# Optimization experiments

Measured on AMD Instinct MI355X. Metric: run time of the kernel, lower is better.

Reference implementation:

```python
import jax, jax.numpy as jnp
import numpy as np
from jax import lax

B, T, C, H, W = 8, 2048, 128, 256, 16
LN_EPS = 1e-5


def setup_inputs() -> dict:
    key = jax.random.key(0)
    ks = jax.random.split(key, 8)
    s_ih = 1.0 / np.sqrt(H)
    return {
        "x": jax.random.normal(ks[0], (B, T, C), jnp.float32),
        "w_ih": jax.random.uniform(ks[1], (3 * H, C), jnp.float32, -s_ih, s_ih),
        "w_hh": jax.random.uniform(ks[2], (3 * H, H), jnp.float32, -s_ih, s_ih),
        "b_ih": jax.random.uniform(ks[3], (3 * H,), jnp.float32, -s_ih, s_ih),
        "b_hh": jax.random.uniform(ks[4], (3 * H,), jnp.float32, -s_ih, s_ih),
        "w_proj": jax.random.normal(ks[5], (H, H), jnp.float32) * (1.0 / np.sqrt(H)),
        "b_proj": jnp.zeros((H,), jnp.float32),
        "ln_gamma": jnp.ones((H,), jnp.float32),
        "ln_beta": jnp.zeros((H,), jnp.float32),
    }


def _sliding_gru(x, w_ih, w_hh, b_ih, b_hh):
    # x: [B,T,C]. Equivalent to running a GRU over each length-W left-padded
    # window ending at t, for all t, returning the final hidden state [B,T,H].
    pad = W - 1
    x_pad = jnp.pad(x, ((0, 0), (pad, 0), (0, 0)))  # [B, T+W-1, C]
    # Precompute input projection once (avoids the [B,T,W,C] unfold buffer).
    xi = jnp.einsum("btc,gc->btg", x_pad, w_ih) + b_ih  # [B, T+W-1, 3H]

    def step(h, w):
        # window step w sees x_pad[:, w : w+T, :] -> precomputed gates slice
        gi = lax.dynamic_slice_in_dim(xi, w, T, axis=1)  # [B,T,3H]
        gh = jnp.einsum("bth,gh->btg", h, w_hh) + b_hh   # [B,T,3H]
        gi_r, gi_z, gi_n = jnp.split(gi, 3, axis=-1)
        gh_r, gh_z, gh_n = jnp.split(gh, 3, axis=-1)
        r = jax.nn.sigmoid(gi_r + gh_r)
        z = jax.nn.sigmoid(gi_z + gh_z)
        n = jnp.tanh(gi_n + r * gh_n)
        h_new = (1.0 - z) * n + z * h
        return h_new, None

    h0 = jnp.zeros((B, T, H), x.dtype)
    h_final, _ = lax.scan(step, h0, jnp.arange(W))
    return h_final  # [B,T,H]


def reference(x, w_ih, w_hh, b_ih, b_hh, w_proj, b_proj, ln_gamma, ln_beta):
    feats = _sliding_gru(x, w_ih, w_hh, b_ih, b_hh)  # [B,T,H]
    y = jnp.einsum("bth,oh->bto", feats, w_proj) + b_proj
    mu = jnp.mean(y, axis=-1, keepdims=True)
    var = jnp.mean(jnp.square(y - mu), axis=-1, keepdims=True)
    y = (y - mu) * lax.rsqrt(var + LN_EPS) * ln_gamma + ln_beta
    return jax.nn.gelu(y, approximate=False)  # dropout is identity in eval
```

## Files before the change

kernel.cpp:

```cpp
#include <hip/hip_runtime.h>
#include <math.h>

typedef unsigned short u16;
typedef unsigned int   u32;
typedef __attribute__((ext_vector_type(8)))  short short8;
typedef __attribute__((ext_vector_type(16))) float f32x16;

#define NT 2048
#define NC 128
#define NH 256
#define NW 16
#define TPAD 2063

#define WS_GI_OFF 720896
#define WS_NEEDED (WS_GI_OFF + (size_t)8 * TPAD * 256 * 8)

__device__ __forceinline__ u16 f2bf(float f) {
  u32 u = __builtin_bit_cast(u32, f);
  u = u + 0x7fffu + ((u >> 16) & 1u);
  return (u16)(u >> 16);
}
__device__ __forceinline__ float bf2f(u16 v) {
  return __builtin_bit_cast(float, (u32)v << 16);
}
__device__ __forceinline__ float bflo(u32 w) {
  return __builtin_bit_cast(float, w << 16);
}
__device__ __forceinline__ float bfhi(u32 w) {
  return __builtin_bit_cast(float, w & 0xffff0000u);
}
__device__ __forceinline__ float nclamp(float v) {
  return fminf(fmaxf(v, -30.0f), 30.0f);
}
__device__ __forceinline__ float fsig(float x) {
  return __builtin_amdgcn_rcpf(1.0f + __builtin_amdgcn_exp2f(-1.44269504f * x));
}
__device__ __forceinline__ float ftanhf(float x) {
  float e = __builtin_amdgcn_exp2f(2.88539008f * x);
  return 1.0f - 2.0f * __builtin_amdgcn_rcpf(e + 1.0f);
}
__device__ __forceinline__ float gelu(float v) {
  return 0.5f * v * (1.0f + erff(v * 0.70710678118654752f));
}

__global__ void pack_w(const float* __restrict__ whh, const float* __restrict__ wih,
                       const float* __restrict__ wpr,
                       u16* __restrict__ whh_p, u16* __restrict__ wih_p,
                       u16* __restrict__ wpr_p) {
  int t = blockIdx.x * 256 + threadIdx.x;
  u16 v[8];
  if (t < 24576) {
    int lane = t & 63, kit = (t >> 6) & 15, nt = t >> 10;
    int wv = nt / 3, g = nt - wv * 3;
    int grow = g * 256 + wv * 32 + (lane & 31);
    int kb = kit * 16 + (lane >> 5) * 8;
    #pragma unroll
    for (int e = 0; e < 8; ++e) v[e] = f2bf(whh[grow * 256 + kb + e]);
    u32* d = (u32*)(whh_p + (size_t)t * 8);
    #pragma unroll
    for (int e = 0; e < 4; ++e) d[e] = (u32)v[2*e] | ((u32)v[2*e+1] << 16);
  } else if (t < 36864) {
    int t2 = t - 24576;
    int lane = t2 & 63, kit = (t2 >> 6) & 7, nt = t2 >> 9;
    int wv = nt / 3, g = nt - wv * 3;
    int grow = g * 256 + wv * 32 + (lane & 31);
    int kb = kit * 16 + (lane >> 5) * 8;
    #pragma unroll
    for (int e = 0; e < 8; ++e) v[e] = f2bf(wih[grow * 128 + kb + e]);
    u32* d = (u32*)(wih_p + (size_t)t2 * 8);
    #pragma unroll
    for (int e = 0; e < 4; ++e) d[e] = (u32)v[2*e] | ((u32)v[2*e+1] << 16);
  } else if (t < 45056) {
    int t3 = t - 36864;
    int lane = t3 & 63, kit = (t3 >> 6) & 15, nt = t3 >> 10;
    int o = nt * 32 + (lane & 31);
    int kb = kit * 16 + (lane >> 5) * 8;
    #pragma unroll
    for (int e = 0; e < 8; ++e) v[e] = f2bf(wpr[o * 256 + kb + e]);
    u32* d = (u32*)(wpr_p + (size_t)t3 * 8);
    #pragma unroll
    for (int e = 0; e < 4; ++e) d[e] = (u32)v[2*e] | ((u32)v[2*e+1] << 16);
  }
}

__global__ __launch_bounds__(512, 2) void xi_kernel(
    const float* __restrict__ x, const float* __restrict__ b_ih,
    const u16* __restrict__ wih_p, uint2* __restrict__ gi) {
  __shared__ u16 xs[64 * 128];
  const int tid = threadIdx.x, wv = tid >> 6, lane = tid & 63;
  const int ml = lane & 31, lh = lane >> 5;
  const int b = blockIdx.x / 33, chunk = blockIdx.x % 33;
  const int tp0 = chunk * 64;
  const int j = wv * 32 + ml;

  {
    int r = tid >> 3, c0e = (tid & 7) * 16;
    int xr = tp0 + r - (NW - 1);
    float vv[16];
    if (xr >= 0 && xr < NT) {
      const float4* src = (const float4*)(x + ((long)b * NT + xr) * NC + c0e);
      #pragma unroll
      for (int q = 0; q < 4; ++q) {
        float4 f = src[q];
        vv[q*4+0] = f.x; vv[q*4+1] = f.y; vv[q*4+2] = f.z; vv[q*4+3] = f.w;
      }
    } else {
      #pragma unroll
      for (int q = 0; q < 16; ++q) vv[q] = 0.0f;
    }
    int byb = r * 256 + c0e * 2;
    int sw = (r & 15) << 4;
    #pragma unroll
    for (int ch = 0; ch < 2; ++ch) {
      u32 q0 = (u32)f2bf(vv[ch*8+0]) | ((u32)f2bf(vv[ch*8+1]) << 16);
      u32 q1 = (u32)f2bf(vv[ch*8+2]) | ((u32)f2bf(vv[ch*8+3]) << 16);
      u32 q2 = (u32)f2bf(vv[ch*8+4]) | ((u32)f2bf(vv[ch*8+5]) << 16);
      u32 q3 = (u32)f2bf(vv[ch*8+6]) | ((u32)f2bf(vv[ch*8+7]) << 16);
      *(uint4*)((char*)xs + ((byb + ch * 16) ^ sw)) = make_uint4(q0, q1, q2, q3);
    }
  }
  __syncthreads();

  const float bi0 = b_ih[j], bi1 = b_ih[NH + j], bi2 = b_ih[2 * NH + j];
  f32x16 acc[2][3];
  #pragma unroll
  for (int mt = 0; mt < 2; ++mt) {
    #pragma unroll
    for (int e = 0; e < 16; ++e) {
      acc[mt][0][e] = bi0; acc[mt][1][e] = bi1; acc[mt][2][e] = bi2;
    }
  }

  const int sw0 = (ml & 15) << 4;
  #pragma unroll 4
  for (int kit = 0; kit < 8; ++kit) {
    short8 a0 = *(const short8*)((const char*)xs +
                  ((ml * 256 + kit * 32 + lh * 16) ^ sw0));
    short8 a1 = *(const short8*)((const char*)xs +
                  (((ml + 32) * 256 + kit * 32 + lh * 16) ^ sw0));
    #pragma unroll
    for (int g = 0; g < 3; ++g) {
      short8 bfr = __builtin_bit_cast(short8,
                     ((const uint4*)wih_p)[((wv * 3 + g) * 8 + kit) * 64 + lane]);
      acc[0][g] = __builtin_amdgcn_mfma_f32_32x32x16_bf16(a0, bfr, acc[0][g], 0, 0, 0);
      acc[1][g] = __builtin_amdgcn_mfma_f32_32x32x16_bf16(a1, bfr, acc[1][g], 0, 0, 0);
    }
  }

  #pragma unroll
  for (int mt = 0; mt < 2; ++mt) {
    #pragma unroll
    for (int rg = 0; rg < 16; ++rg) {
      int m = mt * 32 + (rg & 3) + 8 * (rg >> 2) + 4 * lh;
      int tp = tp0 + m;
      if (tp < TPAD) {
        u32 rz = (u32)f2bf(acc[mt][0][rg]) | ((u32)f2bf(acc[mt][1][rg]) << 16);
        u32 nn = (u32)f2bf(acc[mt][2][rg]);
        gi[((long)b * TPAD + tp) * 256 + j] = make_uint2(rz, nn);
      }
    }
  }
}

__global__ __launch_bounds__(512, 2) void gru_main(
    const float* __restrict__ b_hh,
    const u16* __restrict__ whh_p, const u16* __restrict__ wpr_p,
    const uint2* __restrict__ gi,
    const float* __restrict__ c256_0, const float* __restrict__ c256_1,
    const float* __restrict__ c256_2, float* __restrict__ out) {
  __shared__ u32 rz_lds[79 * 256];
  __shared__ u16 n_lds[79 * 256];
  __shared__ u16 hbuf[64 * 256];
  const int tid = threadIdx.x, wv = tid >> 6, lane = tid & 63;
  const int ml = lane & 31, lh = lane >> 5;
  const int wg = (blockIdx.x & 7) * 32 + (blockIdx.x >> 3);
  const int bidx = wg >> 5, t0 = (wg & 31) * 64;
  const long R0 = (long)wg * 64;
  const int j = wv * 32 + ml;

  const float *gp, *bpp, *bep;
  {
    float v0 = c256_0[0], v1 = c256_1[0];
    if (fabsf(v0 - 1.0f) < 0.25f)      { gp = c256_0; bpp = c256_1; bep = c256_2; }
    else if (fabsf(v1 - 1.0f) < 0.25f) { gp = c256_1; bpp = c256_0; bep = c256_2; }
    else                               { gp = c256_2; bpp = c256_0; bep = c256_1; }
  }

  const float bhr = b_hh[j], bhz = b_hh[NH + j], bnh = b_hh[2 * NH + j];

  {
    const uint2* gwin = gi + ((long)bidx * TPAD + t0) * 256;
    for (int idx = tid; idx < 79 * 256; idx += 512) {
      uint2 v = gwin[idx];
      rz_lds[idx] = v.x;
      n_lds[idx] = (u16)v.y;
    }
  }
  __syncthreads();

  float hreg[2][16];
  #pragma unroll
  for (int mt = 0; mt < 2; ++mt)
    #pragma unroll
    for (int rg = 0; rg < 16; ++rg) hreg[mt][rg] = 0.0f;

  const int swh = (ml & 15) << 4;

  for (int s = 0; s < NW; ++s) {
    f32x16 acc[2][3];
    #pragma unroll
    for (int mt = 0; mt < 2; ++mt) {
      #pragma unroll
      for (int e = 0; e < 16; ++e) {
        acc[mt][0][e] = bhr; acc[mt][1][e] = bhz; acc[mt][2][e] = bnh;
      }
    }

    if (s > 0) {
      #pragma unroll 4
      for (int kit = 0; kit < 16; ++kit) {
        short8 a0 = *(const short8*)((const char*)hbuf +
                      ((ml * 512 + kit * 32 + lh * 16) ^ swh));
        short8 a1 = *(const short8*)((const char*)hbuf +
                      (((ml + 32) * 512 + kit * 32 + lh * 16) ^ swh));
        #pragma unroll
        for (int g = 0; g < 3; ++g) {
          short8 bfr = __builtin_bit_cast(short8,
                         ((const uint4*)whh_p)[(((wv * 3 + g) * 16) + kit) * 64 + lane]);
          acc[0][g] = __builtin_amdgcn_mfma_f32_32x32x16_bf16(a0, bfr, acc[0][g], 0, 0, 0);
          acc[1][g] = __builtin_amdgcn_mfma_f32_32x32x16_bf16(a1, bfr, acc[1][g], 0, 0, 0);
        }
      }
    }
    __syncthreads();

    #pragma unroll
    for (int mt = 0; mt < 2; ++mt) {
      #pragma unroll
      for (int rg = 0; rg < 16; ++rg) {
        int m = mt * 32 + (rg & 3) + 8 * (rg >> 2) + 4 * lh;
        int ro = (s + m) * 256 + j;
        u32 rzv = rz_lds[ro];
        float gnv = bf2f(n_lds[ro]);
        float r = fsig(nclamp(bflo(rzv) + acc[mt][0][rg]));
        float z = fsig(nclamp(bfhi(rzv) + acc[mt][1][rg]));
        float n = ftanhf(nclamp(gnv + r * acc[mt][2][rg]));
        float hv = n + z * (hreg[mt][rg] - n);
        hreg[mt][rg] = hv;
        *(u16*)((char*)hbuf + ((m * 512 + j * 2) ^ ((m & 15) << 4))) = f2bf(hv);
      }
    }
    __syncthreads();
  }

  f32x16 pc[2];
  #pragma unroll
  for (int mt = 0; mt < 2; ++mt)
    #pragma unroll
    for (int e = 0; e < 16; ++e) pc[mt][e] = 0.0f;
  #pragma unroll 4
  for (int kit = 0; kit < 16; ++kit) {
    short8 a0 = *(const short8*)((const char*)hbuf +
                  ((ml * 512 + kit * 32 + lh * 16) ^ swh));
    short8 a1 = *(const short8*)((const char*)hbuf +
                  (((ml + 32) * 512 + kit * 32 + lh * 16) ^ swh));
    short8 bfr = __builtin_bit_cast(short8,
                   ((const uint4*)wpr_p)[(wv * 16 + kit) * 64 + lane]);
    pc[0] = __builtin_amdgcn_mfma_f32_32x32x16_bf16(a0, bfr, pc[0], 0, 0, 0);
    pc[1] = __builtin_amdgcn_mfma_f32_32x32x16_bf16(a1, bfr, pc[1], 0, 0, 0);
  }
  const float bp = bpp[j];
  __syncthreads();
  #pragma unroll
  for (int mt = 0; mt < 2; ++mt) {
    #pragma unroll
    for (int rg = 0; rg < 16; ++rg) {
      int m = mt * 32 + (rg & 3) + 8 * (rg >> 2) + 4 * lh;
      *(u16*)((char*)hbuf + ((m * 512 + j * 2) ^ ((m & 15) << 4))) = f2bf(pc[mt][rg] + bp);
    }
  }
  __syncthreads();

  {
    int m = tid >> 3, cg = (tid & 7) * 32;
    int sw = (m & 15) << 4;
    float v[32];
    #pragma unroll
    for (int q = 0; q < 4; ++q) {
      uint4 raw = *(const uint4*)((char*)hbuf + ((m * 512 + cg * 2 + q * 16) ^ sw));
      u32 w4[4] = {raw.x, raw.y, raw.z, raw.w};
      #pragma unroll
      for (int e = 0; e < 4; ++e) {
        v[q * 8 + e * 2]     = bflo(w4[e]);
        v[q * 8 + e * 2 + 1] = bfhi(w4[e]);
      }
    }
    float s1 = 0.0f, s2 = 0.0f;
    #pragma unroll
    for (int i = 0; i < 32; ++i) { s1 += v[i]; s2 += v[i] * v[i]; }
    #pragma unroll
    for (int d = 1; d < 8; d <<= 1) {
      s1 += __shfl_xor(s1, d, 64);
      s2 += __shfl_xor(s2, d, 64);
    }
    float mu = s1 * (1.0f / 256.0f);
    float var = s2 * (1.0f / 256.0f) - mu * mu;
    if (!(var > 0.0f)) var = 0.0f;
    float rstd = rsqrtf(var + 1e-5f);
    float* od = out + (R0 + m) * NH + cg;
    #pragma unroll
    for (int q = 0; q < 8; ++q) {
      int i0 = q * 4;
      float o0 = gelu((v[i0]     - mu) * rstd * gp[cg + i0]     + bep[cg + i0]);
      float o1 = gelu((v[i0 + 1] - mu) * rstd * gp[cg + i0 + 1] + bep[cg + i0 + 1]);
      float o2 = gelu((v[i0 + 2] - mu) * rstd * gp[cg + i0 + 2] + bep[cg + i0 + 2]);
      float o3 = gelu((v[i0 + 3] - mu) * rstd * gp[cg + i0 + 3] + bep[cg + i0 + 3]);
      *(float4*)(od + i0) = make_float4(o0, o1, o2, o3);
    }
  }
}

__device__ __forceinline__ short8 cvt8(const float* p) {
  float4 a = *(const float4*)p, b = *(const float4*)(p + 4);
  u16 v0 = f2bf(a.x), v1 = f2bf(a.y), v2 = f2bf(a.z), v3 = f2bf(a.w);
  u16 v4 = f2bf(b.x), v5 = f2bf(b.y), v6 = f2bf(b.z), v7 = f2bf(b.w);
  u32 r0 = (u32)v0 | ((u32)v1 << 16), r1 = (u32)v2 | ((u32)v3 << 16);
  u32 r2 = (u32)v4 | ((u32)v5 << 16), r3 = (u32)v6 | ((u32)v7 << 16);
  uint4 r = make_uint4(r0, r1, r2, r3);
  return __builtin_bit_cast(short8, r);
}

__global__ __launch_bounds__(512, 2) void gru_fb(
    const float* __restrict__ x, const float* __restrict__ b_ih, const float* __restrict__ b_hh,
    const float* __restrict__ wih, const float* __restrict__ whh, const float* __restrict__ wpr,
    const float* __restrict__ c256_0, const float* __restrict__ c256_1,
    const float* __restrict__ c256_2, float* __restrict__ out) {
  __shared__ u16 xs[80 * 128];
  __shared__ u16 hb[2][64 * 256];
  const int tid = threadIdx.x, wv = tid >> 6, lane = tid & 63;
  const int ml = lane & 31, lh = lane >> 5;
  const int wg = blockIdx.x;
  const int bidx = wg >> 5, t0 = (wg & 31) * 64;
  const long R0 = (long)wg * 64;
  const int j = wv * 32 + ml;
  const float *gp, *bpp, *bep;
  {
    float v0 = c256_0[0], v1 = c256_1[0];
    if (fabsf(v0 - 1.0f) < 0.25f)      { gp = c256_0; bpp = c256_1; bep = c256_2; }
    else if (fabsf(v1 - 1.0f) < 0.25f) { gp = c256_1; bpp = c256_0; bep = c256_2; }
    else                               { gp = c256_2; bpp = c256_0; bep = c256_1; }
  }
  const float br  = b_ih[j] + b_hh[j];
  const float bz  = b_ih[NH + j] + b_hh[NH + j];
  const float bni = b_ih[2 * NH + j];
  const float bnh = b_hh[2 * NH + j];
  {
    int r = tid >> 3, c0e = (tid & 7) * 16;
    #pragma unroll
    for (int pass = 0; pass < 2; ++pass) {
      int rr = r + pass * 64;
      if (rr < 79) {
        int tx = t0 + rr - (NW - 1);
        float vv[16];
        if (tx >= 0) {
          const float4* src = (const float4*)(x + ((long)bidx * NT + tx) * NC + c0e);
          #pragma unroll
          for (int q = 0; q < 4; ++q) {
            float4 f = src[q];
            vv[q*4+0] = f.x; vv[q*4+1] = f.y; vv[q*4+2] = f.z; vv[q*4+3] = f.w;
          }
        } else {
          #pragma unroll
          for (int q = 0; q < 16; ++q) vv[q] = 0.0f;
        }
        int byb = rr * 256 + c0e * 2;
        int sw = (rr & 15) << 4;
        #pragma unroll
        for (int ch = 0; ch < 2; ++ch) {
          u32 q0 = (u32)f2bf(vv[ch*8+0]) | ((u32)f2bf(vv[ch*8+1]) << 16);
          u32 q1 = (u32)f2bf(vv[ch*8+2]) | ((u32)f2bf(vv[ch*8+3]) << 16);
          u32 q2 = (u32)f2bf(vv[ch*8+4]) | ((u32)f2bf(vv[ch*8+5]) << 16);
          u32 q3 = (u32)f2bf(vv[ch*8+6]) | ((u32)f2bf(vv[ch*8+7]) << 16);
          *(uint4*)((char*)xs + ((byb + ch * 16) ^ sw)) = make_uint4(q0, q1, q2, q3);
        }
      }
    }
  }
  __syncthreads();
  float hreg[2][16];
  #pragma unroll
  for (int mt = 0; mt < 2; ++mt)
    #pragma unroll
    for (int rg = 0; rg < 16; ++rg) hreg[mt][rg] = 0.0f;
  const int swh = (ml & 15) << 4;
  for (int s = 0; s < NW; ++s) {
    f32x16 acc[2][4];
    #pragma unroll
    for (int mt = 0; mt < 2; ++mt)
      #pragma unroll
      for (int g = 0; g < 4; ++g)
        #pragma unroll
        for (int e = 0; e < 16; ++e) acc[mt][g][e] = 0.0f;
    if (s > 0) {
      const u16* hc = hb[(s + 1) & 1];
      #pragma unroll 4
      for (int kit = 0; kit < 16; ++kit) {
        short8 a0 = *(const short8*)((const char*)hc +
                      ((ml * 512 + kit * 32 + lh * 16) ^ swh));
        short8 a1 = *(const short8*)((const char*)hc +
                      (((ml + 32) * 512 + kit * 32 + lh * 16) ^ swh));
        #pragma unroll
        for (int g = 0; g < 3; ++g) {
          short8 bfr = cvt8(whh + (g * 256 + wv * 32 + ml) * 256 + kit * 16 + lh * 8);
          const int ga = (g == 2) ? 3 : g;
          acc[0][ga] = __builtin_amdgcn_mfma_f32_32x32x16_bf16(a0, bfr, acc[0][ga], 0, 0, 0);
          acc[1][ga] = __builtin_amdgcn_mfma_f32_32x32x16_bf16(a1, bfr, acc[1][ga], 0, 0, 0);
        }
      }
    }
    {
      int r0 = s + ml;
      int sw0 = (r0 & 15) << 4;
      #pragma unroll 4
      for (int kit = 0; kit < 8; ++kit) {
        short8 a0 = *(const short8*)((const char*)xs +
                      ((r0 * 256 + kit * 32 + lh * 16) ^ sw0));
        short8 a1 = *(const short8*)((const char*)xs +
                      (((r0 + 32) * 256 + kit * 32 + lh * 16) ^ sw0));
        #pragma unroll
        for (int g = 0; g < 3; ++g) {
          short8 bfr = cvt8(wih + (g * 256 + wv * 32 + ml) * 128 + kit * 16 + lh * 8);
          acc[0][g] = __builtin_amdgcn_mfma_f32_32x32x16_bf16(a0, bfr, acc[0][g], 0, 0, 0);
          acc[1][g] = __builtin_amdgcn_mfma_f32_32x32x16_bf16(a1, bfr, acc[1][g], 0, 0, 0);
        }
      }
    }
    u16* hn = hb[s & 1];
    #pragma unroll
    for (int mt = 0; mt < 2; ++mt) {
      #pragma unroll
      for (int rg = 0; rg < 16; ++rg) {
        int m = mt * 32 + (rg & 3) + 8 * (rg >> 2) + 4 * lh;
        float r = fsig(nclamp(acc[mt][0][rg] + br));
        float z = fsig(nclamp(acc[mt][1][rg] + bz));
        float n = ftanhf(nclamp(acc[mt][2][rg] + bni + r * (acc[mt][3][rg] + bnh)));
        float hv = n + z * (hreg[mt][rg] - n);
        hreg[mt][rg] = hv;
        *(u16*)((char*)hn + ((m * 512 + j * 2) ^ ((m & 15) << 4))) = f2bf(hv);
      }
    }
    __syncthreads();
  }
  f32x16 pc[2];
  #pragma unroll
  for (int mt = 0; mt < 2; ++mt)
    #pragma unroll
    for (int e = 0; e < 16; ++e) pc[mt][e] = 0.0f;
  const u16* hf = hb[1];
  #pragma unroll 4
  for (int kit = 0; kit < 16; ++kit) {
    short8 a0 = *(const short8*)((const char*)hf +
                  ((ml * 512 + kit * 32 + lh * 16) ^ swh));
    short8 a1 = *(const short8*)((const char*)hf +
                  (((ml + 32) * 512 + kit * 32 + lh * 16) ^ swh));
    short8 bfr = cvt8(wpr + (wv * 32 + ml) * 256 + kit * 16 + lh * 8);
    pc[0] = __builtin_amdgcn_mfma_f32_32x32x16_bf16(a0, bfr, pc[0], 0, 0, 0);
    pc[1] = __builtin_amdgcn_mfma_f32_32x32x16_bf16(a1, bfr, pc[1], 0, 0, 0);
  }
  const float bp = bpp[j];
  #pragma unroll
  for (int mt = 0; mt < 2; ++mt) {
    #pragma unroll
    for (int rg = 0; rg < 16; ++rg) {
      int m = mt * 32 + (rg & 3) + 8 * (rg >> 2) + 4 * lh;
      *(u16*)((char*)hb[0] + ((m * 512 + j * 2) ^ ((m & 15) << 4))) = f2bf(pc[mt][rg] + bp);
    }
  }
  __syncthreads();
  {
    int m = tid >> 3, cg = (tid & 7) * 32;
    int sw = (m & 15) << 4;
    float v[32];
    #pragma unroll
    for (int q = 0; q < 4; ++q) {
      uint4 raw = *(const uint4*)((char*)hb[0] + ((m * 512 + cg * 2 + q * 16) ^ sw));
      u32 w4[4] = {raw.x, raw.y, raw.z, raw.w};
      #pragma unroll
      for (int e = 0; e < 4; ++e) {
        v[q * 8 + e * 2]     = bflo(w4[e]);
        v[q * 8 + e * 2 + 1] = bfhi(w4[e]);
      }
    }
    float s1 = 0.0f, s2 = 0.0f;
    #pragma unroll
    for (int i = 0; i < 32; ++i) { s1 += v[i]; s2 += v[i] * v[i]; }
    #pragma unroll
    for (int d = 1; d < 8; d <<= 1) {
      s1 += __shfl_xor(s1, d, 64);
      s2 += __shfl_xor(s2, d, 64);
    }
    float mu = s1 * (1.0f / 256.0f);
    float var = s2 * (1.0f / 256.0f) - mu * mu;
    if (!(var > 0.0f)) var = 0.0f;
    float rstd = rsqrtf(var + 1e-5f);
    float* od = out + (R0 + m) * NH + cg;
    #pragma unroll
    for (int q = 0; q < 8; ++q) {
      int i0 = q * 4;
      float o0 = gelu((v[i0]     - mu) * rstd * gp[cg + i0]     + bep[cg + i0]);
      float o1 = gelu((v[i0 + 1] - mu) * rstd * gp[cg + i0 + 1] + bep[cg + i0 + 1]);
      float o2 = gelu((v[i0 + 2] - mu) * rstd * gp[cg + i0 + 2] + bep[cg + i0 + 2]);
      float o3 = gelu((v[i0 + 3] - mu) * rstd * gp[cg + i0 + 3] + bep[cg + i0 + 3]);
      *(float4*)(od + i0) = make_float4(o0, o1, o2, o3);
    }
  }
}

extern "C" void kernel_launch(void* const* d_in, const int* in_sizes, int n_in,
                              void* d_out, int out_size, void* d_ws, size_t ws_size,
                              hipStream_t stream) {
  (void)out_size;
  const float *x = nullptr, *wih = nullptr, *whh = nullptr, *b768a = nullptr,
              *b768b = nullptr, *wpr = nullptr, *c0 = nullptr, *c1 = nullptr,
              *c2 = nullptr;
  int n768 = 0, n256 = 0;
  for (int i = 0; i < n_in; ++i) {
    const float* p = (const float*)d_in[i];
    switch (in_sizes[i]) {
      case 2097152: x = p; break;
      case 98304:   wih = p; break;
      case 196608:  whh = p; break;
      case 65536:   wpr = p; break;
      case 768:     { if (n768 == 0) b768a = p; else b768b = p; ++n768; } break;
      case 256:     { if (n256 == 0) c0 = p; else if (n256 == 1) c1 = p; else c2 = p; ++n256; } break;
      default: break;
    }
  }
  char* ws = (char*)d_ws;
  u16* whh_p = (u16*)(ws + 0);
  u16* wih_p = (u16*)(ws + 393216);
  u16* wpr_p = (u16*)(ws + 589824);
  uint2* gi  = (uint2*)(ws + WS_GI_OFF);
  float* outp = (float*)d_out;

  if (ws_size >= WS_NEEDED) {
    pack_w<<<dim3(176), dim3(256), 0, stream>>>(whh, wih, wpr, whh_p, wih_p, wpr_p);
    xi_kernel<<<dim3(264), dim3(512), 0, stream>>>(x, b768a, wih_p, gi);
    gru_main<<<dim3(256), dim3(512), 0, stream>>>(b768b, whh_p, wpr_p, gi,
                                                  c0, c1, c2, outp);
  } else {
    gru_fb<<<dim3(256), dim3(512), 0, stream>>>(x, b768a, b768b, wih, whh, wpr,
                                                c0, c1, c2, outp);
  }
}
```

Measured before the change: 205.3 us.

## Double gru_main block to 1024 threads, one M-tile per wave

The recurrent GRU kernel now launches 1024 threads per block and gives each wave a single 32-row M-tile instead of two. This halves the MFMA, gate and LayerNorm work done serially by each wave and doubles the waves available to hide latency. The input clamps before the sigmoid and tanh are also dropped. The launch bound (1024,4) may push the compiler to a very tight VGPR budget and cause spills, and removing the clamps could change behaviour on extreme inputs.

```diff
diff --git a/kernel.cpp b/kernel.cpp
--- a/kernel.cpp
+++ b/kernel.cpp
@@ -162,7 +162,7 @@
   }
 }
 
-__global__ __launch_bounds__(512, 2) void gru_main(
+__global__ __launch_bounds__(1024, 4) void gru_main(
     const float* __restrict__ b_hh,
     const u16* __restrict__ whh_p, const u16* __restrict__ wpr_p,
     const uint2* __restrict__ gi,
@@ -171,12 +171,14 @@
   __shared__ u32 rz_lds[79 * 256];
   __shared__ u16 n_lds[79 * 256];
   __shared__ u16 hbuf[64 * 256];
-  const int tid = threadIdx.x, wv = tid >> 6, lane = tid & 63;
+  const int tid = threadIdx.x, wv4 = tid >> 6, lane = tid & 63;
   const int ml = lane & 31, lh = lane >> 5;
+  const int mt = wv4 >> 3, wvg = wv4 & 7;
   const int wg = (blockIdx.x & 7) * 32 + (blockIdx.x >> 3);
   const int bidx = wg >> 5, t0 = (wg & 31) * 64;
   const long R0 = (long)wg * 64;
-  const int j = wv * 32 + ml;
+  const int j = wvg * 32 + ml;
+  const int arow = mt * 32 + ml;
 
   const float *gp, *bpp, *bep;
   {
@@ -190,7 +192,7 @@
 
   {
     const uint2* gwin = gi + ((long)bidx * TPAD + t0) * 256;
-    for (int idx = tid; idx < 79 * 256; idx += 512) {
+    for (int idx = tid; idx < 79 * 256; idx += 1024) {
       uint2 v = gwin[idx];
       rz_lds[idx] = v.x;
       n_lds[idx] = (u16)v.y;
@@ -198,95 +200,76 @@
   }
   __syncthreads();
 
-  float hreg[2][16];
-  #pragma unroll
-  for (int mt = 0; mt < 2; ++mt)
-    #pragma unroll
-    for (int rg = 0; rg < 16; ++rg) hreg[mt][rg] = 0.0f;
+  float hreg[16];
+  #pragma unroll
+  for (int rg = 0; rg < 16; ++rg) hreg[rg] = 0.0f;
 
   const int swh = (ml & 15) << 4;
 
   for (int s = 0; s < NW; ++s) {
-    f32x16 acc[2][3];
-    #pragma unroll
-    for (int mt = 0; mt < 2; ++mt) {
-      #pragma unroll
-      for (int e = 0; e < 16; ++e) {
-        acc[mt][0][e] = bhr; acc[mt][1][e] = bhz; acc[mt][2][e] = bnh;
-      }
+    f32x16 acc[3];
+    #pragma unroll
+    for (int e = 0; e < 16; ++e) {
+      acc[0][e] = bhr; acc[1][e] = bhz; acc[2][e] = bnh;
     }
 
     if (s > 0) {
       #pragma unroll 4
       for (int kit = 0; kit < 16; ++kit) {
         short8 a0 = *(const short8*)((const char*)hbuf +
-                      ((ml * 512 + kit * 32 + lh * 16) ^ swh));
-        short8 a1 = *(const short8*)((const char*)hbuf +
-                      (((ml + 32) * 512 + kit * 32 + lh * 16) ^ swh));
+                      ((arow * 512 + kit * 32 + lh * 16) ^ swh));
         #pragma unroll
         for (int g = 0; g < 3; ++g) {
           short8 bfr = __builtin_bit_cast(short8,
-                         ((const uint4*)whh_p)[(((wv * 3 + g) * 16) + kit) * 64 + lane]);
-          acc[0][g] = __builtin_amdgcn_mfma_f32_32x32x16_bf16(a0, bfr, acc[0][g], 0, 0, 0);
-          acc[1][g] = __builtin_amdgcn_mfma_f32_32x32x16_bf16(a1, bfr, acc[1][g], 0, 0, 0);
+                         ((const uint4*)whh_p)[(((wvg * 3 + g) * 16) + kit) * 64 + lane]);
+          acc[g] = __builtin_amdgcn_mfma_f32_32x32x16_bf16(a0, bfr, acc[g], 0, 0, 0);
         }
       }
     }
     __syncthreads();
 
     #pragma unroll
-    for (int mt = 0; mt < 2; ++mt) {
-      #pragma unroll
-      for (int rg = 0; rg < 16; ++rg) {
-        int m = mt * 32 + (rg & 3) + 8 * (rg >> 2) + 4 * lh;
-        int ro = (s + m) * 256 + j;
-        u32 rzv = rz_lds[ro];
-        float gnv = bf2f(n_lds[ro]);
-        float r = fsig(nclamp(bflo(rzv) + acc[mt][0][rg]));
-        float z = fsig(nclamp(bfhi(rzv) + acc[mt][1][rg]));
-        float n = ftanhf(nclamp(gnv + r * acc[mt][2][rg]));
-        float hv = n + z * (hreg[mt][rg] - n);
-        hreg[mt][rg] = hv;
-        *(u16*)((char*)hbuf + ((m * 512 + j * 2) ^ ((m & 15) << 4))) = f2bf(hv);
-      }
+    for (int rg = 0; rg < 16; ++rg) {
+      int m = mt * 32 + (rg & 3) + 8 * (rg >> 2) + 4 * lh;
+      int ro = (s + m) * 256 + j;
+      u32 rzv = rz_lds[ro];
+      float gnv = bf2f(n_lds[ro]);
+      float r = fsig(bflo(rzv) + acc[0][rg]);
+      float z = fsig(bfhi(rzv) + acc[1][rg]);
+      float n = ftanhf(gnv + r * acc[2][rg]);
+      float hv = n + z * (hreg[rg] - n);
+      hreg[rg] = hv;
+      *(u16*)((char*)hbuf + ((m * 512 + j * 2) ^ ((m & 15) << 4))) = f2bf(hv);
     }
     __syncthreads();
   }
 
-  f32x16 pc[2];
-  #pragma unroll
-  for (int mt = 0; mt < 2; ++mt)
-    #pragma unroll
-    for (int e = 0; e < 16; ++e) pc[mt][e] = 0.0f;
+  f32x16 pc;
+  #pragma unroll
+  for (int e = 0; e < 16; ++e) pc[e] = 0.0f;
   #pragma unroll 4
   for (int kit = 0; kit < 16; ++kit) {
     short8 a0 = *(const short8*)((const char*)hbuf +
-                  ((ml * 512 + kit * 32 + lh * 16) ^ swh));
-    short8 a1 = *(const short8*)((const char*)hbuf +
-                  (((ml + 32) * 512 + kit * 32 + lh * 16) ^ swh));
+                  ((arow * 512 + kit * 32 + lh * 16) ^ swh));
     short8 bfr = __builtin_bit_cast(short8,
-                   ((const uint4*)wpr_p)[(wv * 16 + kit) * 64 + lane]);
-    pc[0] = __builtin_amdgcn_mfma_f32_32x32x16_bf16(a0, bfr, pc[0], 0, 0, 0);
-    pc[1] = __builtin_amdgcn_mfma_f32_32x32x16_bf16(a1, bfr, pc[1], 0, 0, 0);
+                   ((const uint4*)wpr_p)[(wvg * 16 + kit) * 64 + lane]);
+    pc = __builtin_amdgcn_mfma_f32_32x32x16_bf16(a0, bfr, pc, 0, 0, 0);
   }
   const float bp = bpp[j];
   __syncthreads();
   #pragma unroll
-  for (int mt = 0; mt < 2; ++mt) {
-    #pragma unroll
-    for (int rg = 0; rg < 16; ++rg) {
-      int m = mt * 32 + (rg & 3) + 8 * (rg >> 2) + 4 * lh;
-      *(u16*)((char*)hbuf + ((m * 512 + j * 2) ^ ((m & 15) << 4))) = f2bf(pc[mt][rg] + bp);
-    }
+  for (int rg = 0; rg < 16; ++rg) {
+    int m = mt * 32 + (rg & 3) + 8 * (rg >> 2) + 4 * lh;
+    *(u16*)((char*)hbuf + ((m * 512 + j * 2) ^ ((m & 15) << 4))) = f2bf(pc[rg] + bp);
   }
   __syncthreads();
 
   {
-    int m = tid >> 3, cg = (tid & 7) * 32;
+    int m = tid >> 4, cg = (tid & 15) * 16;
     int sw = (m & 15) << 4;
-    float v[32];
-    #pragma unroll
-    for (int q = 0; q < 4; ++q) {
+    float v[16];
+    #pragma unroll
+    for (int q = 0; q < 2; ++q) {
       uint4 raw = *(const uint4*)((char*)hbuf + ((m * 512 + cg * 2 + q * 16) ^ sw));
       u32 w4[4] = {raw.x, raw.y, raw.z, raw.w};
       #pragma unroll
@@ -297,9 +280,9 @@
     }
     float s1 = 0.0f, s2 = 0.0f;
     #pragma unroll
-    for (int i = 0; i < 32; ++i) { s1 += v[i]; s2 += v[i] * v[i]; }
-    #pragma unroll
-    for (int d = 1; d < 8; d <<= 1) {
+    for (int i = 0; i < 16; ++i) { s1 += v[i]; s2 += v[i] * v[i]; }
+    #pragma unroll
+    for (int d = 1; d < 16; d <<= 1) {
       s1 += __shfl_xor(s1, d, 64);
       s2 += __shfl_xor(s2, d, 64);
     }
@@ -309,7 +292,7 @@
     float rstd = rsqrtf(var + 1e-5f);
     float* od = out + (R0 + m) * NH + cg;
     #pragma unroll
-    for (int q = 0; q < 8; ++q) {
+    for (int q = 0; q < 4; ++q) {
       int i0 = q * 4;
       float o0 = gelu((v[i0]     - mu) * rstd * gp[cg + i0]     + bep[cg + i0]);
       float o1 = gelu((v[i0 + 1] - mu) * rstd * gp[cg + i0 + 1] + bep[cg + i0 + 1]);
@@ -546,8 +529,8 @@
   if (ws_size >= WS_NEEDED) {
     pack_w<<<dim3(176), dim3(256), 0, stream>>>(whh, wih, wpr, whh_p, wih_p, wpr_p);
     xi_kernel<<<dim3(264), dim3(512), 0, stream>>>(x, b768a, wih_p, gi);
-    gru_main<<<dim3(256), dim3(512), 0, stream>>>(b768b, whh_p, wpr_p, gi,
-                                                  c0, c1, c2, outp);
+    gru_main<<<dim3(256), dim3(1024), 0, stream>>>(b768b, whh_p, wpr_p, gi,
+                                                   c0, c1, c2, outp);
   } else {
     gru_fb<<<dim3(256), dim3(512), 0, stream>>>(x, b768a, b768b, wih, whh, wpr,
                                                 c0, c1, c2, outp);
```

Result: slower. 210.4 us (+2.5%).
